# Kernel tuning notes

Measured on AMD Instinct MI355X. Metric: run time of the kernel, lower is better.

The kernel has to match this reference:

```python
import jax, jax.numpy as jnp
import numpy as np

N_SRC = 131072
N_DST = 65536
N_EDGES = 524288
D_IN = 128
D_OUT = 128


def setup_inputs() -> dict:
    key = jax.random.key(0)
    k1, k2, k3, k4, k5 = jax.random.split(key, 5)
    feat = jax.random.normal(k1, (N_SRC, D_IN), dtype=jnp.float32)
    # xavier_uniform-ish scale for the two projections
    lim = float(np.sqrt(6.0 / (D_IN + D_OUT))) * np.sqrt(2.0)
    W_self = jax.random.uniform(k2, (D_IN, D_OUT), jnp.float32, -lim, lim)
    W_neigh = jax.random.uniform(k3, (D_IN, D_OUT), jnp.float32, -lim, lim)
    b_self = jnp.zeros((D_OUT,), jnp.float32)
    b_neigh = jnp.zeros((D_OUT,), jnp.float32)
    src_idx = jax.random.randint(k4, (N_EDGES,), 0, N_SRC, dtype=jnp.int32)
    dst_idx = jnp.sort(jax.random.randint(k5, (N_EDGES,), 0, N_DST, dtype=jnp.int32))
    return {
        "feat": feat,
        "W_self": W_self,
        "b_self": b_self,
        "W_neigh": W_neigh,
        "b_neigh": b_neigh,
        "src_idx": src_idx,
        "dst_idx": dst_idx,
        "num_row": N_DST,
    }


def reference(feat, W_self, b_self, W_neigh, b_neigh, src_idx, dst_idx, num_row):
    # h_self: destination-node features (first num_row rows)
    h_self = feat[:num_row, :]                              # [num_row, D_IN]
    # csrmm: mean aggregation of source neighbor features per destination row
    gathered = feat[src_idx]                                # [E, D_IN]
    neigh_sum = jax.ops.segment_sum(gathered, dst_idx, num_segments=num_row)
    deg = jax.ops.segment_sum(jnp.ones_like(dst_idx, dtype=feat.dtype), dst_idx,
                              num_segments=num_row)
    h_neigh = neigh_sum / jnp.maximum(deg, 1.0)[:, None]    # [num_row, D_IN]
    # dual linear projections
    rst = (h_self @ W_self + b_self) + (h_neigh @ W_neigh + b_neigh)
    return rst
```

## Files before the change

### kernel.cpp

```cpp
#include <hip/hip_runtime.h>
#include <hip/hip_bf16.h>

#define N_SRC   131072
#define N_DST   65536
#define D       128

typedef __bf16 bf16x8 __attribute__((ext_vector_type(8)));
typedef float  f32x4  __attribute__((ext_vector_type(4)));

#define CONV_BLOCKS 8192
#define W_BLOCKS    64

__global__ __launch_bounds__(256) void prep_kernel(
    const float* __restrict__ feat,
    const int*   __restrict__ dst, int n_edges, int n_bnd_blocks,
    const float* __restrict__ W_self, const float* __restrict__ W_neigh,
    __bf16* __restrict__ feat_bf,
    int*    __restrict__ row_start,
    __bf16* __restrict__ Wt_self, __bf16* __restrict__ Wt_neigh)
{
    const int b = blockIdx.x;
    const int t = threadIdx.x;

    if (b < CONV_BLOCKS) {
        const size_t i0 = ((size_t)b * 256 + t) * 8;
        const float4 a0 = *(const float4*)&feat[i0];
        const float4 a1 = *(const float4*)&feat[i0 + 4];
        bf16x8 o;
        o[0] = (__bf16)a0.x; o[1] = (__bf16)a0.y; o[2] = (__bf16)a0.z; o[3] = (__bf16)a0.w;
        o[4] = (__bf16)a1.x; o[5] = (__bf16)a1.y; o[6] = (__bf16)a1.z; o[7] = (__bf16)a1.w;
        *(bf16x8*)&feat_bf[i0] = o;
    } else if (b < CONV_BLOCKS + n_bnd_blocks) {
        const int e = (b - CONV_BLOCKS) * 256 + t;
        if (e < n_edges) {
            const int d    = dst[e];
            const int prev = (e == 0) ? -1 : dst[e - 1];
            for (int r = prev + 1; r <= d; ++r) row_start[r] = e;
            if (e == n_edges - 1)
                for (int r = d + 1; r <= N_DST; ++r) row_start[r] = n_edges;
        }
    } else {
        const int wb  = b - CONV_BLOCKS - n_bnd_blocks;
        const int idx = wb * 256 + t;
        const int k = idx >> 7, n = idx & 127;
        Wt_self [n * D + k] = (__bf16)W_self [k * D + n];
        Wt_neigh[n * D + k] = (__bf16)W_neigh[k * D + n];
    }
}

#define MTILE 128
#define MREP  2

__global__ __launch_bounds__(256) void fused_kernel(
    const __bf16* __restrict__ feat_bf,
    const int*    __restrict__ src,
    const int*    __restrict__ row_start,
    const __bf16* __restrict__ Wt_self,
    const __bf16* __restrict__ Wt_neigh,
    const float*  __restrict__ b_self,
    const float*  __restrict__ b_neigh,
    float*        __restrict__ out)
{
    __shared__ __align__(16) __bf16 hs[MTILE * D];
    char* hsb = (char*)hs;

    const int t     = threadIdx.x;
    const int tile0 = blockIdx.x * MTILE;

    {
        const int g    = t >> 4;
        const int lane = t & 15;
        const int cb   = lane * 16;

        #pragma unroll
        for (int rr = 0; rr < MTILE / 16; ++rr) {
            const int rloc = rr * 16 + g;
            const int s0 = row_start[tile0 + rloc];
            const int s1 = row_start[tile0 + rloc + 1];

            float acc[8] = {0.f, 0.f, 0.f, 0.f, 0.f, 0.f, 0.f, 0.f};

            for (int base = s0; base < s1; base += 8) {
                int idx[8];
                #pragma unroll
                for (int j = 0; j < 8; ++j) {
                    const int e = base + j;
                    idx[j] = src[e < s1 ? e : s1 - 1];
                }
                bf16x8 v[8];
                #pragma unroll
                for (int j = 0; j < 8; ++j)
                    v[j] = *(const bf16x8*)((const char*)feat_bf + (size_t)idx[j] * (D * 2) + cb);
                #pragma unroll
                for (int j = 0; j < 8; ++j) {
                    const float m = (base + j < s1) ? 1.0f : 0.0f;
                    #pragma unroll
                    for (int c = 0; c < 8; ++c)
                        acc[c] = fmaf(m, (float)v[j][c], acc[c]);
                }
            }

            const float inv = 1.0f / fmaxf((float)(s1 - s0), 1.0f);
            bf16x8 o;
            #pragma unroll
            for (int c = 0; c < 8; ++c) o[c] = (__bf16)(acc[c] * inv);
            *(bf16x8*)(hsb + rloc * 256 + (cb ^ ((rloc & 7) << 4))) = o;
        }
    }

    const int w    = t >> 6;
    const int l    = t & 63;
    const int m16  = l & 15;
    const int quad = l >> 4;
    const int kb   = quad * 8;
    const int rowloc0 = w * (16 * MREP);
    const int rowbase = tile0 + rowloc0;

    f32x4 acc[MREP][8];
    #pragma unroll
    for (int rp = 0; rp < MREP; ++rp)
        #pragma unroll
        for (int nb = 0; nb < 8; ++nb)
            acc[rp][nb] = (f32x4){0.f, 0.f, 0.f, 0.f};

    #pragma unroll
    for (int ks = 0; ks < 4; ++ks) {
        bf16x8 afrag[MREP];
        #pragma unroll
        for (int rp = 0; rp < MREP; ++rp)
            afrag[rp] = *(const bf16x8*)&feat_bf[(size_t)(rowbase + rp * 16 + m16) * D + ks * 32 + kb];
        #pragma unroll
        for (int nb = 0; nb < 8; ++nb) {
            const bf16x8 bfrag = *(const bf16x8*)&Wt_self[(size_t)(nb * 16 + m16) * D + ks * 32 + kb];
            #pragma unroll
            for (int rp = 0; rp < MREP; ++rp)
                acc[rp][nb] = __builtin_amdgcn_mfma_f32_16x16x32_bf16(
                    afrag[rp], bfrag, acc[rp][nb], 0, 0, 0);
        }
    }

    __syncthreads();

    #pragma unroll
    for (int ks = 0; ks < 4; ++ks) {
        bf16x8 afrag[MREP];
        #pragma unroll
        for (int rp = 0; rp < MREP; ++rp) {
            const int rloc  = rowloc0 + rp * 16 + m16;
            const int cbyte = (ks * 32 + kb) * 2;
            afrag[rp] = *(const bf16x8*)(hsb + rloc * 256 + (cbyte ^ ((rloc & 7) << 4)));
        }
        #pragma unroll
        for (int nb = 0; nb < 8; ++nb) {
            const bf16x8 bfrag = *(const bf16x8*)&Wt_neigh[(size_t)(nb * 16 + m16) * D + ks * 32 + kb];
            #pragma unroll
            for (int rp = 0; rp < MREP; ++rp)
                acc[rp][nb] = __builtin_amdgcn_mfma_f32_16x16x32_bf16(
                    afrag[rp], bfrag, acc[rp][nb], 0, 0, 0);
        }
    }

    #pragma unroll
    for (int nb = 0; nb < 8; ++nb) {
        const int col  = nb * 16 + m16;
        const float bias = b_self[col] + b_neigh[col];
        #pragma unroll
        for (int rp = 0; rp < MREP; ++rp) {
            const int orow0 = rowbase + rp * 16 + quad * 4;
            #pragma unroll
            for (int r = 0; r < 4; ++r)
                out[(size_t)(orow0 + r) * D + col] = acc[rp][nb][r] + bias;
        }
    }
}

extern "C" void kernel_launch(void* const* d_in, const int* in_sizes, int n_in,
                              void* d_out, int out_size, void* d_ws, size_t ws_size,
                              hipStream_t stream)
{
    const float* feat    = (const float*)d_in[0];
    const float* W_self  = (const float*)d_in[1];
    const float* b_self  = (const float*)d_in[2];
    const float* W_neigh = (const float*)d_in[3];
    const float* b_neigh = (const float*)d_in[4];
    const int*   src_idx = (const int*)d_in[5];
    const int*   dst_idx = (const int*)d_in[6];
    const int n_edges = in_sizes[5];

    char* ws = (char*)d_ws;
    __bf16* feat_bf  = (__bf16*)ws;
    int*    row_start = (int*)(feat_bf + (size_t)N_SRC * D);
    __bf16* Wt_self  = (__bf16*)(row_start + N_DST + 16);
    __bf16* Wt_neigh = Wt_self + D * D;

    const int n_bnd = (n_edges + 255) / 256;
    prep_kernel<<<CONV_BLOCKS + n_bnd + W_BLOCKS, 256, 0, stream>>>(
        feat, dst_idx, n_edges, n_bnd, W_self, W_neigh,
        feat_bf, row_start, Wt_self, Wt_neigh);

    fused_kernel<<<N_DST / MTILE, 256, 0, stream>>>(
        feat_bf, src_idx, row_start, Wt_self, Wt_neigh,
        b_self, b_neigh, (float*)d_out);
}
```

Baseline: 160.1 us.

## Halve tile to 64 rows, raise occupancy, prefetch self-features before gather

Shrinks the per-block destination tile from 128 to 64 rows, which doubles the grid to 1024 blocks and removes the MREP register replication. The launch bound asks for 4 blocks per SM. Self-feature A fragments are now loaded at kernel start, so their latency overlaps the neighbor gather. The aim is more waves in flight to hide gather latency. The cost is that each W fragment load now feeds only one MFMA, so W is reloaded twice as often, and the early-loaded fragments stay live in registers during the gather.

Measured after the change: 170.8 us. 6.7% more time.

```diff
diff --git a/kernel.cpp b/kernel.cpp
--- a/kernel.cpp
+++ b/kernel.cpp
@@ -48,10 +48,9 @@
     }
 }
 
-#define MTILE 128
-#define MREP  2
+#define MTILE 64
 
-__global__ __launch_bounds__(256) void fused_kernel(
+__global__ __launch_bounds__(256, 4) void fused_kernel(
     const __bf16* __restrict__ feat_bf,
     const int*    __restrict__ src,
     const int*    __restrict__ row_start,
@@ -66,6 +65,19 @@
 
     const int t     = threadIdx.x;
     const int tile0 = blockIdx.x * MTILE;
+
+    const int w    = t >> 6;
+    const int l    = t & 63;
+    const int m16  = l & 15;
+    const int quad = l >> 4;
+    const int kb   = quad * 8;
+    const int rowloc0 = w * 16;
+    const int rowbase = tile0 + rowloc0;
+
+    bf16x8 aself[4];
+    #pragma unroll
+    for (int ks = 0; ks < 4; ++ks)
+        aself[ks] = *(const bf16x8*)&feat_bf[(size_t)(rowbase + m16) * D + ks * 32 + kb];
 
     {
         const int g    = t >> 4;
@@ -108,34 +120,18 @@
         }
     }
 
-    const int w    = t >> 6;
-    const int l    = t & 63;
-    const int m16  = l & 15;
-    const int quad = l >> 4;
-    const int kb   = quad * 8;
-    const int rowloc0 = w * (16 * MREP);
-    const int rowbase = tile0 + rowloc0;
-
-    f32x4 acc[MREP][8];
+    f32x4 acc[8];
     #pragma unroll
-    for (int rp = 0; rp < MREP; ++rp)
-        #pragma unroll
-        for (int nb = 0; nb < 8; ++nb)
-            acc[rp][nb] = (f32x4){0.f, 0.f, 0.f, 0.f};
+    for (int nb = 0; nb < 8; ++nb)
+        acc[nb] = (f32x4){0.f, 0.f, 0.f, 0.f};
 
     #pragma unroll
     for (int ks = 0; ks < 4; ++ks) {
-        bf16x8 afrag[MREP];
-        #pragma unroll
-        for (int rp = 0; rp < MREP; ++rp)
-            afrag[rp] = *(const bf16x8*)&feat_bf[(size_t)(rowbase + rp * 16 + m16) * D + ks * 32 + kb];
         #pragma unroll
         for (int nb = 0; nb < 8; ++nb) {
             const bf16x8 bfrag = *(const bf16x8*)&Wt_self[(size_t)(nb * 16 + m16) * D + ks * 32 + kb];
-            #pragma unroll
-            for (int rp = 0; rp < MREP; ++rp)
-                acc[rp][nb] = __builtin_amdgcn_mfma_f32_16x16x32_bf16(
-                    afrag[rp], bfrag, acc[rp][nb], 0, 0, 0);
+            acc[nb] = __builtin_amdgcn_mfma_f32_16x16x32_bf16(
+                aself[ks], bfrag, acc[nb], 0, 0, 0);
         }
     }
 
@@ -143,20 +139,14 @@
 
     #pragma unroll
     for (int ks = 0; ks < 4; ++ks) {
-        bf16x8 afrag[MREP];
-        #pragma unroll
-        for (int rp = 0; rp < MREP; ++rp) {
-            const int rloc  = rowloc0 + rp * 16 + m16;
-            const int cbyte = (ks * 32 + kb) * 2;
-            afrag[rp] = *(const bf16x8*)(hsb + rloc * 256 + (cbyte ^ ((rloc & 7) << 4)));
-        }
+        const int rloc  = rowloc0 + m16;
+        const int cbyte = (ks * 32 + kb) * 2;
+        const bf16x8 afrag = *(const bf16x8*)(hsb + rloc * 256 + (cbyte ^ ((rloc & 7) << 4)));
         #pragma unroll
         for (int nb = 0; nb < 8; ++nb) {
             const bf16x8 bfrag = *(const bf16x8*)&Wt_neigh[(size_t)(nb * 16 + m16) * D + ks * 32 + kb];
-            #pragma unroll
-            for (int rp = 0; rp < MREP; ++rp)
-                acc[rp][nb] = __builtin_amdgcn_mfma_f32_16x16x32_bf16(
-                    afrag[rp], bfrag, acc[rp][nb], 0, 0, 0);
+            acc[nb] = __builtin_amdgcn_mfma_f32_16x16x32_bf16(
+                afrag, bfrag, acc[nb], 0, 0, 0);
         }
     }
 
@@ -164,13 +154,10 @@
     for (int nb = 0; nb < 8; ++nb) {
         const int col  = nb * 16 + m16;
         const float bias = b_self[col] + b_neigh[col];
+        const int orow0 = rowbase + quad * 4;
         #pragma unroll
-        for (int rp = 0; rp < MREP; ++rp) {
-            const int orow0 = rowbase + rp * 16 + quad * 4;
-            #pragma unroll
-            for (int r = 0; r < 4; ++r)
-                out[(size_t)(orow0 + r) * D + col] = acc[rp][nb][r] + bias;
-        }
+        for (int r = 0; r < 4; ++r)
+            out[(size_t)(orow0 + r) * D + col] = acc[nb][r] + bias;
     }
 }
 
```
